# Kernel optimization log

Hardware: AMD Instinct MI355X
Metric: run time of the kernel (lower is better)

## Reference

```python
import jax, jax.numpy as jnp
import numpy as np

N_NODES = 100000
N_EDGES = 1600000
IN_DIM = 128
EMB = 64
HID = 2 * EMB  # 128


def gcn_conv(x, W, b, row, col, norm):
    # PyG GCNConv: h = x @ W, then aggregate norm-weighted messages src->dst, then +bias
    h = x @ W                                   # [N, out]
    msg = norm[:, None] * h[row]                # gather over source nodes [E', out]
    out = jax.ops.segment_sum(msg, col, num_segments=N_NODES)  # scatter to targets
    return out + b


def gcn_norm(edge_index, edge_weight, n_nodes):
    # add self-loops with weight 1, then symmetric normalization D^-1/2 A D^-1/2
    loop = jnp.arange(n_nodes, dtype=edge_index.dtype)
    row = jnp.concatenate([edge_index[0], loop])
    col = jnp.concatenate([edge_index[1], loop])
    ew = jnp.concatenate([edge_weight, jnp.ones((n_nodes,), edge_weight.dtype)])
    deg = jax.ops.segment_sum(ew, col, num_segments=n_nodes)
    dinv = jnp.where(deg > 0, jax.lax.rsqrt(deg), 0.0)
    norm = dinv[row] * ew * dinv[col]
    return row, col, norm


def setup_inputs() -> dict:
    key = jax.random.key(0)
    ks = jax.random.split(key, 10)
    x = jax.random.normal(ks[0], (N_NODES, IN_DIM), dtype=jnp.float32)
    edge_index = jax.random.randint(ks[1], (2, N_EDGES), 0, N_NODES, dtype=jnp.int64)
    edge_weight = jax.random.uniform(ks[2], (N_EDGES,), dtype=jnp.float32)
    s1 = 1.0 / np.sqrt(IN_DIM)
    s2 = 1.0 / np.sqrt(HID)
    W1 = jax.random.uniform(ks[3], (IN_DIM, HID), jnp.float32, -s1, s1)
    b1 = jnp.zeros((HID,), jnp.float32)
    Wmu = jax.random.uniform(ks[4], (HID, EMB), jnp.float32, -s2, s2)
    bmu = jnp.zeros((EMB,), jnp.float32)
    Wlv = jax.random.uniform(ks[5], (HID, EMB), jnp.float32, -s2, s2)
    blv = jnp.zeros((EMB,), jnp.float32)
    return {"x": x, "edge_index": edge_index, "edge_weight": edge_weight,
            "W1": W1, "b1": b1, "Wmu": Wmu, "bmu": bmu, "Wlv": Wlv, "blv": blv}


def reference(x, edge_index, edge_weight, W1, b1, Wmu, bmu, Wlv, blv):
    row, col, norm = gcn_norm(edge_index, edge_weight, N_NODES)
    h = jax.nn.relu(gcn_conv(x, W1, b1, row, col, norm))
    mu = gcn_conv(h, Wmu, bmu, row, col, norm)
    logvar = gcn_conv(h, Wlv, blv, row, col, norm)
    return (mu, logvar)
```

## Files before the change

### kernel.cpp

```cpp
#include <hip/hip_runtime.h>

#define NN 100000
#define NE 1600000
#define DD 128
#define OUT_HALF 6400000
#define CAP 64

#define NB 256
#define NPB 391
#define BCAP 8192
#define BSTRIDE 64
#define CHUNK 2048
#define CPT 8

#define GNM 64
#define XPITCH 140

typedef unsigned int uint_t;
typedef float v4f __attribute__((ext_vector_type(4)));
typedef short v8s __attribute__((ext_vector_type(8)));

__device__ __forceinline__ unsigned short f2bf(float f) {
    uint_t u = __float_as_uint(f);
    u = (u + 0x7fffu + ((u >> 16) & 1u)) >> 16;
    return (unsigned short)u;
}
__device__ __forceinline__ float bf2f(unsigned short h) {
    return __uint_as_float(((uint_t)h) << 16);
}
__device__ __forceinline__ float bf_lo(uint_t u) { return __uint_as_float(u << 16); }
__device__ __forceinline__ float bf_hi(uint_t u) { return __uint_as_float(u & 0xffff0000u); }

#define EW_SCALE 32767.0f
#define EW_INV (1.0f / 32767.0f)


__global__ void k_zero(int* __restrict__ bcnt) {
    int i = blockIdx.x * blockDim.x + threadIdx.x;
    if (i < NB * BSTRIDE) bcnt[i] = 0;
}

__launch_bounds__(256)
__global__ void k_bin(const int* __restrict__ row, const int* __restrict__ col,
                      const float* __restrict__ ew, int* __restrict__ bcnt,
                      uint2* __restrict__ bins) {
    __shared__ uint2 sorted[CHUNK];
    __shared__ int hist[NB];
    __shared__ int lstart[NB];
    __shared__ int offs[NB];
    __shared__ int gbase[NB];
    const int tid = threadIdx.x;
    const int ebase = blockIdx.x * CHUNK;
    const int nloc = (NE - ebase < CHUNK) ? (NE - ebase) : CHUNK;

    hist[tid] = 0;
    __syncthreads();

    uint_t cols[CPT];
#pragma unroll
    for (int k = 0; k < CPT; ++k) {
        int i = ebase + k * 256 + tid;
        cols[k] = (i < NE) ? (uint_t)col[i] : 0xffffffffu;
        if (i < NE) atomicAdd(&hist[cols[k] / NPB], 1);
    }
    __syncthreads();

    int v = hist[tid];
#pragma unroll
    for (int s = 1; s < NB; s <<= 1) {
        int t = (tid >= s) ? hist[tid - s] : 0;
        __syncthreads();
        hist[tid] += t;
        __syncthreads();
    }
    int excl = hist[tid] - v;
    lstart[tid] = excl;
    offs[tid] = excl;
    gbase[tid] = atomicAdd(&bcnt[tid * BSTRIDE], v);
    __syncthreads();

#pragma unroll
    for (int k = 0; k < CPT; ++k) {
        int i = ebase + k * 256 + tid;
        if (i < NE) {
            uint_t c = cols[k];
            uint_t r = (uint_t)row[i];
            uint_t q = (uint_t)__float2int_rn(ew[i] * EW_SCALE);
            int pos = atomicAdd(&offs[c / NPB], 1);
            sorted[pos] = make_uint2((r << 15) | q, c);
        }
    }
    __syncthreads();

    for (int i = tid; i < nloc; i += 256) {
        uint2 rec = sorted[i];
        uint_t b = rec.y / NPB;
        int dst = gbase[b] + (i - lstart[b]);
        if (dst < BCAP) bins[(size_t)b * BCAP + dst] = rec;
    }
}


__launch_bounds__(512)
__global__ void k_scatter(const int* __restrict__ bcnt, const uint2* __restrict__ bins,
                          int* __restrict__ cnt, uint_t* __restrict__ slots,
                          float* __restrict__ dinv) {
    __shared__ int combo[NPB];
    const int b = blockIdx.x;
    const int tid = threadIdx.x;
    if (tid < NPB) combo[tid] = 0;
    __syncthreads();
    int n = bcnt[b * BSTRIDE];
    n = (n < BCAP) ? n : BCAP;
    const int base = b * NPB;
    const uint2* seg = bins + (size_t)b * BCAP;
    for (int i = tid; i < n; i += 512) {
        uint2 rec = seg[i];
        int lc = (int)rec.y - base;
        uint_t w = rec.x & 0x7fffu;
        uint_t old = (uint_t)atomicAdd(&combo[lc], (int)((1u << 22) | w));
        uint_t pos = old >> 22;
        if (pos < CAP) slots[rec.y * CAP + pos] = rec.x;
    }
    __syncthreads();
    if (tid < NPB) {
        int node = base + tid;
        if (node < NN) {
            uint_t v = (uint_t)combo[tid];
            int c = (int)(v >> 22);
            c = (c < CAP) ? c : CAP;
            int cp = (c + 15) & ~15;
            cnt[node] = cp;
            dinv[node] = rsqrtf(1.0f + (float)(v & 0x3fffffu) * EW_INV);
            uint_t padrec = (uint_t)node << 15;
            for (int j = c; j < cp; ++j) slots[node * CAP + j] = padrec;
        }
    }
}


template <bool RELU, bool OUT_BF16>
__launch_bounds__(256)
__global__ void k_gather(const uint_t* __restrict__ src, const int* __restrict__ cnt,
                         const uint_t* __restrict__ slots, const float* __restrict__ dinv,
                         const float* __restrict__ bias, void* __restrict__ dst) {
    int wid = (blockIdx.x * blockDim.x + threadIdx.x) >> 6;
    int lane = threadIdx.x & 63;
    if (wid >= NN) return;
    float di = dinv[wid];
    uint_t u = src[wid * 64 + lane];
    float accx = bf_lo(u);
    float accy = bf_hi(u);
    int end = __builtin_amdgcn_readfirstlane(cnt[wid]);
    const uint_t* seg = slots + wid * CAP;
    for (int jj = 0; jj < end; jj += 16) {
        uint_t rp[16];
#pragma unroll
        for (int q = 0; q < 16; ++q) rp[q] = seg[jj + q];
        uint_t sv[16];
#pragma unroll
        for (int q = 0; q < 16; ++q) sv[q] = src[(rp[q] >> 15) * 64 + lane];
#pragma unroll
        for (int q = 0; q < 16; ++q) {
            float p = (float)(rp[q] & 0x7fffu) * EW_INV;
            accx = fmaf(p, bf_lo(sv[q]), accx);
            accy = fmaf(p, bf_hi(sv[q]), accy);
        }
    }
    accx *= di;
    accy *= di;
    if (RELU) {
        float2 b = ((const float2*)bias)[lane];
        accx = fmaxf(accx + b.x, 0.0f) * di;
        accy = fmaxf(accy + b.y, 0.0f) * di;
    }
    if (OUT_BF16) {
        ((uint_t*)dst)[wid * 64 + lane] =
            (uint_t)f2bf(accx) | ((uint_t)f2bf(accy) << 16);
    } else {
        ((float2*)dst)[wid * 64 + lane] = make_float2(accx, accy);
    }
}


__global__ void k_wpack1(const float* __restrict__ W, unsigned short* __restrict__ P) {
    int e = blockIdx.x * blockDim.x + threadIdx.x;
    if (e >= 2048) return;
    int ln = e & 15, nt = (e >> 4) & 7, la = (e >> 7) & 3, kt = e >> 9;
    v8s v;
#pragma unroll
    for (int j = 0; j < 8; ++j) {
        int k = kt * 32 + la * 4 + (j & 3) + 16 * (j >> 2);
        v[j] = (short)f2bf(W[k * 128 + nt * 16 + ln]);
    }
    *(v8s*)&P[e * 8] = v;
}

__global__ void k_wpack2(const float* __restrict__ Wmu, const float* __restrict__ Wlv,
                         unsigned short* __restrict__ P) {
    int e = blockIdx.x * blockDim.x + threadIdx.x;
    if (e >= 2048) return;
    int ln = e & 15, nt = (e >> 4) & 7, la = (e >> 7) & 3, kt = e >> 9;
    v8s v;
#pragma unroll
    for (int j = 0; j < 8; ++j) {
        int k = kt * 32 + la * 4 + (j & 3) + 16 * (j >> 2);
        float f = (nt < 4) ? Wmu[k * 64 + nt * 16 + ln]
                           : Wlv[k * 64 + (nt - 4) * 16 + ln];
        v[j] = (short)f2bf(f);
    }
    *(v8s*)&P[e * 8] = v;
}


__launch_bounds__(256)
__global__ void k_gemm_h0(const float* __restrict__ X,
                          const unsigned short* __restrict__ Wpk,
                          const float* __restrict__ dinv,
                          unsigned short* __restrict__ Y) {
    __shared__ float xs[GNM * XPITCH];
    const int tid = threadIdx.x;
    const int node0 = blockIdx.x * GNM;

    {
        const float4* X4 = (const float4*)X;
        for (int i = tid; i < GNM * 32; i += 256) {
            int row = i >> 5, kg = i & 31;
            int ne = node0 + row;
            if (ne >= NN) ne = NN - 1;
            *(float4*)&xs[row * XPITCH + kg * 4] = X4[ne * 32 + kg];
        }
    }
    __syncthreads();

    const int wave = tid >> 6, lane = tid & 63;
    const int la = lane >> 4, ln = lane & 15;
    const float* xrow = &xs[(wave * 16 + ln) * XPITCH];
    const v8s* Wf = (const v8s*)Wpk;

    v4f acc[8];
#pragma unroll
    for (int nt = 0; nt < 8; ++nt) acc[nt] = (v4f){0.f, 0.f, 0.f, 0.f};

    for (int kt = 0; kt < 4; ++kt) {
        float4 xa0 = *(const float4*)&xrow[kt * 32 + la * 4];
        float4 xa1 = *(const float4*)&xrow[kt * 32 + la * 4 + 16];
        float xv[8] = {xa0.x, xa0.y, xa0.z, xa0.w, xa1.x, xa1.y, xa1.z, xa1.w};
        v8s ah, al;
#pragma unroll
        for (int j = 0; j < 8; ++j) {
            unsigned short h = f2bf(xv[j]);
            ah[j] = (short)h;
            al[j] = (short)f2bf(xv[j] - bf2f(h));
        }
        const int wbase = (kt * 4 + la) * 8 * 16;
#pragma unroll
        for (int nt = 0; nt < 8; ++nt) {
            v8s bh = Wf[wbase + nt * 16 + ln];
            acc[nt] = __builtin_amdgcn_mfma_f32_16x16x32_bf16(ah, bh, acc[nt], 0, 0, 0);
            acc[nt] = __builtin_amdgcn_mfma_f32_16x16x32_bf16(al, bh, acc[nt], 0, 0, 0);
        }
    }

#pragma unroll
    for (int r = 0; r < 4; ++r) {
        int node = node0 + wave * 16 + la * 4 + r;
        if (node < NN) {
            float di = dinv[node];
#pragma unroll
            for (int nt = 0; nt < 8; ++nt)
                Y[node * 128 + nt * 16 + ln] = f2bf(acc[nt][r] * di);
        }
    }
}


__launch_bounds__(256)
__global__ void k_gg_out(const uint_t* __restrict__ src, const int* __restrict__ cnt,
                         const uint_t* __restrict__ slots, const float* __restrict__ dinv,
                         const unsigned short* __restrict__ Wpk,
                         const float* __restrict__ bmu, const float* __restrict__ blv,
                         float* __restrict__ out) {
    __shared__ float xs[GNM * XPITCH];
    const int tid = threadIdx.x;
    const int node0 = blockIdx.x * GNM;
    const int wave = tid >> 6, lane = tid & 63;

    for (int n = 0; n < 16; ++n) {
        int node = node0 + wave * 16 + n;
        float accx = 0.0f, accy = 0.0f;
        if (node < NN) {
            float di = dinv[node];
            uint_t u = src[node * 64 + lane];
            accx = bf_lo(u);
            accy = bf_hi(u);
            int end = __builtin_amdgcn_readfirstlane(cnt[node]);
            const uint_t* seg = slots + node * CAP;
            for (int jj = 0; jj < end; jj += 16) {
                uint_t rp[16];
#pragma unroll
                for (int q = 0; q < 16; ++q) rp[q] = seg[jj + q];
                uint_t sv[16];
#pragma unroll
                for (int q = 0; q < 16; ++q) sv[q] = src[(rp[q] >> 15) * 64 + lane];
#pragma unroll
                for (int q = 0; q < 16; ++q) {
                    float p = (float)(rp[q] & 0x7fffu) * EW_INV;
                    accx = fmaf(p, bf_lo(sv[q]), accx);
                    accy = fmaf(p, bf_hi(sv[q]), accy);
                }
            }
            accx *= di;
            accy *= di;
        }
        xs[(wave * 16 + n) * XPITCH + lane * 2] = accx;
        xs[(wave * 16 + n) * XPITCH + lane * 2 + 1] = accy;
    }
    __syncthreads();

    const int la = lane >> 4, ln = lane & 15;
    const float* xrow = &xs[(wave * 16 + ln) * XPITCH];
    const v8s* Wf = (const v8s*)Wpk;

    v4f acc[8];
#pragma unroll
    for (int nt = 0; nt < 8; ++nt) acc[nt] = (v4f){0.f, 0.f, 0.f, 0.f};

    for (int kt = 0; kt < 4; ++kt) {
        float4 xa0 = *(const float4*)&xrow[kt * 32 + la * 4];
        float4 xa1 = *(const float4*)&xrow[kt * 32 + la * 4 + 16];
        float xv[8] = {xa0.x, xa0.y, xa0.z, xa0.w, xa1.x, xa1.y, xa1.z, xa1.w};
        v8s ah, al;
#pragma unroll
        for (int j = 0; j < 8; ++j) {
            unsigned short h = f2bf(xv[j]);
            ah[j] = (short)h;
            al[j] = (short)f2bf(xv[j] - bf2f(h));
        }
        const int wbase = (kt * 4 + la) * 8 * 16;
#pragma unroll
        for (int nt = 0; nt < 8; ++nt) {
            v8s bh = Wf[wbase + nt * 16 + ln];
            acc[nt] = __builtin_amdgcn_mfma_f32_16x16x32_bf16(ah, bh, acc[nt], 0, 0, 0);
            acc[nt] = __builtin_amdgcn_mfma_f32_16x16x32_bf16(al, bh, acc[nt], 0, 0, 0);
        }
    }

    float bb[8];
#pragma unroll
    for (int nt = 0; nt < 8; ++nt)
        bb[nt] = (nt < 4) ? bmu[nt * 16 + ln] : blv[(nt - 4) * 16 + ln];

#pragma unroll
    for (int r = 0; r < 4; ++r) {
        int node = node0 + wave * 16 + la * 4 + r;
        if (node < NN) {
#pragma unroll
            for (int nt = 0; nt < 8; ++nt) {
                float v = acc[nt][r] + bb[nt];
                if (nt < 4)
                    out[node * 64 + nt * 16 + ln] = v;
                else
                    out[OUT_HALF + node * 64 + (nt - 4) * 16 + ln] = v;
            }
        }
    }
}


extern "C" void kernel_launch(void* const* d_in, const int* in_sizes, int n_in,
                              void* d_out, int out_size, void* d_ws, size_t ws_size,
                              hipStream_t stream) {
    const float* x   = (const float*)d_in[0];
    const int*   ei  = (const int*)d_in[1];
    const float* ew  = (const float*)d_in[2];
    const float* W1  = (const float*)d_in[3];
    const float* b1  = (const float*)d_in[4];
    const float* Wmu = (const float*)d_in[5];
    const float* bmu = (const float*)d_in[6];
    const float* Wlv = (const float*)d_in[7];
    const float* blv = (const float*)d_in[8];
    const int* rowi = ei;
    const int* coli = ei + NE;
    float* out = (float*)d_out;

    int*    cnt   = (int*)d_ws;
    float*  dinv  = (float*)(cnt + 100352);
    uint_t* slots = (uint_t*)(dinv + 100352);
    float*  poolA = (float*)(slots + NN * CAP);
    uint_t* y0    = (uint_t*)poolA;
    uint_t* y1    = (uint_t*)(poolA + NN * DD);
    uint2*  bins  = (uint2*)poolA;
    int*    bcnt  = (int*)(poolA + NB * BCAP * 2);
    unsigned short* Wpk1 = (unsigned short*)(poolA + NN * 64);
    unsigned short* Wpk2 = (unsigned short*)poolA;

    const int B = 256;
    const int GGRID = (NN + GNM - 1) / GNM;
    k_zero<<<(NB * BSTRIDE + B - 1) / B, B, 0, stream>>>(bcnt);
    k_bin<<<(NE + CHUNK - 1) / CHUNK, B, 0, stream>>>(rowi, coli, ew, bcnt, bins);
    k_scatter<<<NB, 512, 0, stream>>>(bcnt, bins, cnt, slots, dinv);
    k_wpack1<<<8, B, 0, stream>>>(W1, Wpk1);
    k_gemm_h0<<<GGRID, B, 0, stream>>>(x, Wpk1, dinv, (unsigned short*)y0);
    k_gather<true, true><<<(NN * 64 + B - 1) / B, B, 0, stream>>>(
        y0, cnt, slots, dinv, b1, y1);
    k_wpack2<<<8, B, 0, stream>>>(Wmu, Wlv, Wpk2);
    k_gg_out<<<GGRID, B, 0, stream>>>(y1, cnt, slots, dinv, Wpk2, bmu, blv, out);
}
```

Baseline: 317.5 us.

## Merge weight packing and zeroing into one prep kernel, swizzle GEMM LDS tiles

Folds the bin-counter zeroing and both weight-packing kernels into a single prep launch, removing two kernel launches from the sequence. Replaces the padded LDS row pitch in both MFMA GEMM kernels with an XOR-swizzled 128-float layout, which shrinks shared memory per block and is intended to avoid bank conflicts. Adds a minimum-occupancy hint of 5 blocks per CU via launch bounds, which may constrain register allocation. Wpk2 moves to its own workspace location so it can be packed early without being overwritten by the bins buffer.

```diff
diff --git a/kernel.cpp b/kernel.cpp
--- a/kernel.cpp
+++ b/kernel.cpp
@@ -14,7 +14,6 @@
 #define CPT 8
 
 #define GNM 64
-#define XPITCH 140
 
 typedef unsigned int uint_t;
 typedef float v4f __attribute__((ext_vector_type(4)));
@@ -35,10 +34,38 @@
 #define EW_INV (1.0f / 32767.0f)
 
 
-__global__ void k_zero(int* __restrict__ bcnt) {
-    int i = blockIdx.x * blockDim.x + threadIdx.x;
-    if (i < NB * BSTRIDE) bcnt[i] = 0;
-}
+__global__ void k_prep(const float* __restrict__ W1, const float* __restrict__ Wmu,
+                       const float* __restrict__ Wlv, unsigned short* __restrict__ P1,
+                       unsigned short* __restrict__ P2, int* __restrict__ bcnt) {
+    const int b = blockIdx.x, tid = threadIdx.x;
+    if (b < 8) {
+        int e = b * 256 + tid;
+        int ln = e & 15, nt = (e >> 4) & 7, la = (e >> 7) & 3, kt = e >> 9;
+        v8s v;
+#pragma unroll
+        for (int j = 0; j < 8; ++j) {
+            int k = kt * 32 + la * 4 + (j & 3) + 16 * (j >> 2);
+            v[j] = (short)f2bf(W1[k * 128 + nt * 16 + ln]);
+        }
+        *(v8s*)&P1[e * 8] = v;
+    } else if (b < 16) {
+        int e = (b - 8) * 256 + tid;
+        int ln = e & 15, nt = (e >> 4) & 7, la = (e >> 7) & 3, kt = e >> 9;
+        v8s v;
+#pragma unroll
+        for (int j = 0; j < 8; ++j) {
+            int k = kt * 32 + la * 4 + (j & 3) + 16 * (j >> 2);
+            float f = (nt < 4) ? Wmu[k * 64 + nt * 16 + ln]
+                               : Wlv[k * 64 + (nt - 4) * 16 + ln];
+            v[j] = (short)f2bf(f);
+        }
+        *(v8s*)&P2[e * 8] = v;
+    } else {
+        int i = (b - 16) * 256 + tid;
+        if (i < NB * BSTRIDE) bcnt[i] = 0;
+    }
+}
+
 
 __launch_bounds__(256)
 __global__ void k_bin(const int* __restrict__ row, const int* __restrict__ col,
@@ -183,59 +210,31 @@
 }
 
 
-__global__ void k_wpack1(const float* __restrict__ W, unsigned short* __restrict__ P) {
-    int e = blockIdx.x * blockDim.x + threadIdx.x;
-    if (e >= 2048) return;
-    int ln = e & 15, nt = (e >> 4) & 7, la = (e >> 7) & 3, kt = e >> 9;
-    v8s v;
-#pragma unroll
-    for (int j = 0; j < 8; ++j) {
-        int k = kt * 32 + la * 4 + (j & 3) + 16 * (j >> 2);
-        v[j] = (short)f2bf(W[k * 128 + nt * 16 + ln]);
-    }
-    *(v8s*)&P[e * 8] = v;
-}
-
-__global__ void k_wpack2(const float* __restrict__ Wmu, const float* __restrict__ Wlv,
-                         unsigned short* __restrict__ P) {
-    int e = blockIdx.x * blockDim.x + threadIdx.x;
-    if (e >= 2048) return;
-    int ln = e & 15, nt = (e >> 4) & 7, la = (e >> 7) & 3, kt = e >> 9;
-    v8s v;
-#pragma unroll
-    for (int j = 0; j < 8; ++j) {
-        int k = kt * 32 + la * 4 + (j & 3) + 16 * (j >> 2);
-        float f = (nt < 4) ? Wmu[k * 64 + nt * 16 + ln]
-                           : Wlv[k * 64 + (nt - 4) * 16 + ln];
-        v[j] = (short)f2bf(f);
-    }
-    *(v8s*)&P[e * 8] = v;
-}
-
-
-__launch_bounds__(256)
+__launch_bounds__(256, 5)
 __global__ void k_gemm_h0(const float* __restrict__ X,
                           const unsigned short* __restrict__ Wpk,
                           const float* __restrict__ dinv,
                           unsigned short* __restrict__ Y) {
-    __shared__ float xs[GNM * XPITCH];
+    __shared__ float xs[GNM * 128];
     const int tid = threadIdx.x;
     const int node0 = blockIdx.x * GNM;
 
     {
         const float4* X4 = (const float4*)X;
+        float4* xs4 = (float4*)xs;
         for (int i = tid; i < GNM * 32; i += 256) {
             int row = i >> 5, kg = i & 31;
             int ne = node0 + row;
             if (ne >= NN) ne = NN - 1;
-            *(float4*)&xs[row * XPITCH + kg * 4] = X4[ne * 32 + kg];
+            xs4[row * 32 + (kg ^ (row & 7))] = X4[ne * 32 + kg];
         }
     }
     __syncthreads();
 
     const int wave = tid >> 6, lane = tid & 63;
     const int la = lane >> 4, ln = lane & 15;
-    const float* xrow = &xs[(wave * 16 + ln) * XPITCH];
+    const int lx = ln & 7;
+    const float* xrow = &xs[(wave * 16 + ln) * 128];
     const v8s* Wf = (const v8s*)Wpk;
 
     v4f acc[8];
@@ -243,8 +242,8 @@
     for (int nt = 0; nt < 8; ++nt) acc[nt] = (v4f){0.f, 0.f, 0.f, 0.f};
 
     for (int kt = 0; kt < 4; ++kt) {
-        float4 xa0 = *(const float4*)&xrow[kt * 32 + la * 4];
-        float4 xa1 = *(const float4*)&xrow[kt * 32 + la * 4 + 16];
+        float4 xa0 = *(const float4*)&xrow[((kt * 8 + la) ^ lx) << 2];
+        float4 xa1 = *(const float4*)&xrow[((kt * 8 + la + 4) ^ lx) << 2];
         float xv[8] = {xa0.x, xa0.y, xa0.z, xa0.w, xa1.x, xa1.y, xa1.z, xa1.w};
         v8s ah, al;
 #pragma unroll
@@ -275,13 +274,13 @@
 }
 
 
-__launch_bounds__(256)
+__launch_bounds__(256, 5)
 __global__ void k_gg_out(const uint_t* __restrict__ src, const int* __restrict__ cnt,
                          const uint_t* __restrict__ slots, const float* __restrict__ dinv,
                          const unsigned short* __restrict__ Wpk,
                          const float* __restrict__ bmu, const float* __restrict__ blv,
                          float* __restrict__ out) {
-    __shared__ float xs[GNM * XPITCH];
+    __shared__ float xs[GNM * 128];
     const int tid = threadIdx.x;
     const int node0 = blockIdx.x * GNM;
     const int wave = tid >> 6, lane = tid & 63;
@@ -313,13 +312,16 @@
             accx *= di;
             accy *= di;
         }
-        xs[(wave * 16 + n) * XPITCH + lane * 2] = accx;
-        xs[(wave * 16 + n) * XPITCH + lane * 2 + 1] = accy;
+        int r = wave * 16 + n;
+        int f4 = (lane >> 1) ^ (n & 7);
+        *(float2*)&xs[r * 128 + (f4 << 2) + ((lane & 1) << 1)] =
+            make_float2(accx, accy);
     }
     __syncthreads();
 
     const int la = lane >> 4, ln = lane & 15;
-    const float* xrow = &xs[(wave * 16 + ln) * XPITCH];
+    const int lx = ln & 7;
+    const float* xrow = &xs[(wave * 16 + ln) * 128];
     const v8s* Wf = (const v8s*)Wpk;
 
     v4f acc[8];
@@ -327,8 +329,8 @@
     for (int nt = 0; nt < 8; ++nt) acc[nt] = (v4f){0.f, 0.f, 0.f, 0.f};
 
     for (int kt = 0; kt < 4; ++kt) {
-        float4 xa0 = *(const float4*)&xrow[kt * 32 + la * 4];
-        float4 xa1 = *(const float4*)&xrow[kt * 32 + la * 4 + 16];
+        float4 xa0 = *(const float4*)&xrow[((kt * 8 + la) ^ lx) << 2];
+        float4 xa1 = *(const float4*)&xrow[((kt * 8 + la + 4) ^ lx) << 2];
         float xv[8] = {xa0.x, xa0.y, xa0.z, xa0.w, xa1.x, xa1.y, xa1.z, xa1.w};
         v8s ah, al;
 #pragma unroll
@@ -393,17 +395,15 @@
     uint2*  bins  = (uint2*)poolA;
     int*    bcnt  = (int*)(poolA + NB * BCAP * 2);
     unsigned short* Wpk1 = (unsigned short*)(poolA + NN * 64);
-    unsigned short* Wpk2 = (unsigned short*)poolA;
+    unsigned short* Wpk2 = (unsigned short*)(poolA + NN * 64 + 8192);
 
     const int B = 256;
     const int GGRID = (NN + GNM - 1) / GNM;
-    k_zero<<<(NB * BSTRIDE + B - 1) / B, B, 0, stream>>>(bcnt);
+    k_prep<<<80, B, 0, stream>>>(W1, Wmu, Wlv, Wpk1, Wpk2, bcnt);
     k_bin<<<(NE + CHUNK - 1) / CHUNK, B, 0, stream>>>(rowi, coli, ew, bcnt, bins);
     k_scatter<<<NB, 512, 0, stream>>>(bcnt, bins, cnt, slots, dinv);
-    k_wpack1<<<8, B, 0, stream>>>(W1, Wpk1);
     k_gemm_h0<<<GGRID, B, 0, stream>>>(x, Wpk1, dinv, (unsigned short*)y0);
     k_gather<true, true><<<(NN * 64 + B - 1) / B, B, 0, stream>>>(
         y0, cnt, slots, dinv, b1, y1);
-    k_wpack2<<<8, B, 0, stream>>>(Wmu, Wlv, Wpk2);
     k_gg_out<<<GGRID, B, 0, stream>>>(y1, cnt, slots, dinv, Wpk2, bmu, blv, out);
 }
```

After: 314.1 us. About the same (-1.1%).
